# Optimization experiments

Hardware: AMD Instinct MI355X
Metric: run time of the kernel (lower is better)

## Reference

```python
import jax, jax.numpy as jnp
import numpy as np

N_NODES = 50000
N_EDGES = 800000
D_IN = 64
D_OUT = 64
EDGE_DIM = 32
BN_EPS = 1e-5
GIN_EPS = 0.0


def setup_inputs() -> dict:
    key = jax.random.key(0)
    ks = jax.random.split(key, 8)
    x = jax.random.normal(ks[0], (N_NODES, D_IN), dtype=jnp.float32)
    edge_index = jax.random.randint(ks[1], (2, N_EDGES), 0, N_NODES, dtype=jnp.int64)
    edge_attr = jax.random.normal(ks[2], (N_EDGES, EDGE_DIM), dtype=jnp.float32)
    # learned params (scaled like kaiming-ish init)
    We = jax.random.normal(ks[3], (EDGE_DIM, D_IN), dtype=jnp.float32) / np.sqrt(EDGE_DIM)
    be = jnp.zeros((D_IN,), dtype=jnp.float32)
    W1 = jax.random.normal(ks[4], (D_IN, D_OUT), dtype=jnp.float32) / np.sqrt(D_IN)
    b1 = jnp.zeros((D_OUT,), dtype=jnp.float32)
    gamma = jnp.ones((D_OUT,), dtype=jnp.float32)
    beta = jnp.zeros((D_OUT,), dtype=jnp.float32)
    W2 = jax.random.normal(ks[5], (D_OUT, D_OUT), dtype=jnp.float32) / np.sqrt(D_OUT)
    b2 = jnp.zeros((D_OUT,), dtype=jnp.float32)
    return {"x": x, "edge_index": edge_index, "edge_attr": edge_attr,
            "We": We, "be": be, "W1": W1, "b1": b1,
            "gamma": gamma, "beta": beta, "W2": W2, "b2": b2}


def reference(x, edge_index, edge_attr, We, be, W1, b1, gamma, beta, W2, b2):
    src = edge_index[0]  # j (source), PyG default flow source_to_target
    dst = edge_index[1]  # i (target)
    # message: x_j + lin(edge_attr)
    msg = x[src] + (edge_attr @ We + be)              # [E, D_IN]
    # scatter-add aggregate into target nodes
    agg = jax.ops.segment_sum(msg, dst, num_segments=x.shape[0])  # [N, D_IN]
    # GIN residual
    out = agg + (1.0 + GIN_EPS) * x
    # MLP: Linear -> BatchNorm1d (training stats) -> ReLU -> Linear
    h = out @ W1 + b1
    mean = jnp.mean(h, axis=0)
    var = jnp.var(h, axis=0)
    h = (h - mean) * jax.lax.rsqrt(var + BN_EPS) * gamma + beta
    h = jax.nn.relu(h)
    return h @ W2 + b2
```

## Files before the change

### kernel.cpp

```cpp
#include <hip/hip_runtime.h>

#define N_NODES 50000
#define N_EDGES 800000
#define D 64
#define ED 32
#define BN_EPS 1e-5f

#define NBKT 250
#define NPB  200
#define NB_HIST 500
#define EPB  1600

#define WS_SUMS     0
#define WS_SUMSQ    64
#define WS_BTOT     128
#define WS_RESV     384
#define WS_ZERO_END 640
#define WS_OFF      640
#define WS_PACK     50644
#define WS_SRC2     (WS_PACK + 2 * N_EDGES)
#define WS_AGGEA    (WS_SRC2 + 2 * N_EDGES)
#define WS_PRE      (WS_AGGEA + N_NODES * ED)
#define WS_H        (WS_PRE + N_NODES * D)
#define WS_WC       (WS_H + N_NODES * D)
#define WS_BEC      (WS_WC + ED * D)

#define N_BLK ((N_NODES + 63) / 64)

__global__ __launch_bounds__(256) void foldw_kernel(
    const float* __restrict__ We, const float* __restrict__ W1,
    const float* __restrict__ be, float* __restrict__ wc, float* __restrict__ bec)
{
    const int idx = blockIdx.x * 256 + threadIdx.x;
    if (idx < ED * D) {
        const int j = idx >> 6, f = idx & 63;
        float a = 0.f;
        for (int k = 0; k < D; ++k) a += We[j * D + k] * W1[k * D + f];
        wc[idx] = a;
    }
    if (idx < D) {
        float a = 0.f;
        for (int k = 0; k < D; ++k) a += be[k] * W1[k * D + idx];
        bec[idx] = a;
    }
}

__global__ __launch_bounds__(256) void bin_hist_kernel(
    const int* __restrict__ dst, int* __restrict__ btot)
{
    __shared__ int hist[NBKT];
    const int t = threadIdx.x;
    if (t < NBKT) hist[t] = 0;
    __syncthreads();
    const int e0 = blockIdx.x * EPB;
    for (int i = t; i < EPB; i += 256)
        atomicAdd(&hist[dst[e0 + i] / NPB], 1);
    __syncthreads();
    if (t < NBKT) atomicAdd(&btot[t], hist[t]);
}

__global__ __launch_bounds__(256) void bin_scatter_kernel(
    const int* __restrict__ ei, const int* __restrict__ btot,
    int* __restrict__ resv, uint2* __restrict__ pack)
{
    __shared__ int sA[256], sB[256];
    __shared__ int bb[NBKT];
    __shared__ int hist[NBKT], seg[NBKT], lcur[NBKT];
    const int t = threadIdx.x;
    if (t < NBKT) { hist[t] = 0; lcur[t] = 0; }
    sA[t] = (t < NBKT) ? btot[t] : 0;
    __syncthreads();
    int* cur = sA; int* nxt = sB;
    for (int o = 1; o < 256; o <<= 1) {
        nxt[t] = cur[t] + (t >= o ? cur[t - o] : 0);
        __syncthreads();
        int* tmp = cur; cur = nxt; nxt = tmp;
    }
    if (t < NBKT) bb[t] = (t == 0) ? 0 : cur[t - 1];
    __syncthreads();

    const int e0 = blockIdx.x * EPB;
    for (int i = t; i < EPB; i += 256)
        atomicAdd(&hist[ei[N_EDGES + e0 + i] / NPB], 1);
    __syncthreads();
    if (t < NBKT) seg[t] = bb[t] + atomicAdd(&resv[t], hist[t]);
    __syncthreads();
    for (int i = t; i < EPB; i += 256) {
        const int e = e0 + i;
        const int s = ei[e];
        const int d = ei[N_EDGES + e];
        const int bkt = d / NPB;
        const int r = atomicAdd(&lcur[bkt], 1);
        pack[seg[bkt] + r] = make_uint2(((unsigned)d << 16) | (unsigned)s,
                                        (unsigned)e);
    }
}

__global__ __launch_bounds__(512) void bucket_place_kernel(
    const int* __restrict__ btot, const uint2* __restrict__ pack,
    int* __restrict__ off, int2* __restrict__ sorted)
{
    __shared__ int sA[256], sB[256];
    __shared__ int cnt[NPB], lcur[NPB];
    __shared__ int pA[256], pB[256];
    __shared__ int sBase, sNE;
    const int t = threadIdx.x;
    const int j = blockIdx.x;
    if (t < 256) sA[t] = (t < NBKT) ? btot[t] : 0;
    if (t < NPB) { cnt[t] = 0; lcur[t] = 0; }
    __syncthreads();
    int* cur = sA; int* nxt = sB;
    for (int o = 1; o < 256; o <<= 1) {
        if (t < 256) nxt[t] = cur[t] + (t >= o ? cur[t - o] : 0);
        __syncthreads();
        int* tmp = cur; cur = nxt; nxt = tmp;
    }
    if (t == 0) { sBase = (j == 0) ? 0 : cur[j - 1]; sNE = btot[j]; }
    __syncthreads();
    const int base = sBase, nE = sNE;
    const uint2* pp = pack + base;

    for (int i = t; i < nE; i += 512)
        atomicAdd(&cnt[(int)(pp[i].x >> 16) - j * NPB], 1);
    __syncthreads();
    if (t < 256) pA[t] = (t < NPB) ? cnt[t] : 0;
    __syncthreads();
    int* c2 = pA; int* n2 = pB;
    for (int o = 1; o < 256; o <<= 1) {
        if (t < 256) n2[t] = c2[t] + (t >= o ? c2[t - o] : 0);
        __syncthreads();
        int* tmp = c2; c2 = n2; n2 = tmp;
    }
    if (t < NPB) {
        const int excl = (t == 0) ? 0 : c2[t - 1];
        n2[t] = excl;
        off[j * NPB + t] = base + excl;
    }
    if (j == NBKT - 1 && t == 0) off[N_NODES] = N_EDGES;
    __syncthreads();
    for (int i = t; i < nE; i += 512) {
        const uint2 w = pp[i];
        const int dl = (int)(w.x >> 16) - j * NPB;
        const int r = atomicAdd(&lcur[dl], 1);
        sorted[base + n2[dl] + r] = make_int2((int)w.y, (int)(w.x & 0xffffu));
    }
}

__global__ __launch_bounds__(256) void agg_kernel(
    const float* __restrict__ x, const float* __restrict__ ea,
    const int* __restrict__ off, const int2* __restrict__ sorted,
    float* __restrict__ pre, float* __restrict__ aggEA)
{
    const int f = threadIdx.x & 63;
    const int w = threadIdx.x >> 6;
    const int fe = f & 31;
    const bool lo = (f < 32);
    const int nwv = gridDim.x * 4;
    for (int node = blockIdx.x * 4 + w; node < N_NODES; node += nwv) {
        const int start = __builtin_amdgcn_readfirstlane(off[node]);
        const int n     = __builtin_amdgcn_readfirstlane(off[node + 1]) - start;
        const int2* sp = sorted + start;
        float s = x[(size_t)node * D + f];
        float ax = 0.f, ay = 0.f;
        int it = 0;
        if (n >= 8) {
            int2 c0 = sp[0], c1 = sp[1], c2 = sp[2], c3 = sp[3];
            int2 c4 = sp[4], c5 = sp[5], c6 = sp[6], c7 = sp[7];
            for (; it + 16 <= n; it += 8) {
                const int2 n0 = sp[it + 8],  n1 = sp[it + 9];
                const int2 n2 = sp[it + 10], n3 = sp[it + 11];
                const int2 n4 = sp[it + 12], n5 = sp[it + 13];
                const int2 n6 = sp[it + 14], n7 = sp[it + 15];
                s += x[(size_t)c0.y * D + f]; s += x[(size_t)c1.y * D + f];
                s += x[(size_t)c2.y * D + f]; s += x[(size_t)c3.y * D + f];
                s += x[(size_t)c4.y * D + f]; s += x[(size_t)c5.y * D + f];
                s += x[(size_t)c6.y * D + f]; s += x[(size_t)c7.y * D + f];
                ax += ea[(size_t)(lo ? c0.x : c1.x) * ED + fe];
                ax += ea[(size_t)(lo ? c2.x : c3.x) * ED + fe];
                ay += ea[(size_t)(lo ? c4.x : c5.x) * ED + fe];
                ay += ea[(size_t)(lo ? c6.x : c7.x) * ED + fe];
                c0 = n0; c1 = n1; c2 = n2; c3 = n3;
                c4 = n4; c5 = n5; c6 = n6; c7 = n7;
            }
            s += x[(size_t)c0.y * D + f]; s += x[(size_t)c1.y * D + f];
            s += x[(size_t)c2.y * D + f]; s += x[(size_t)c3.y * D + f];
            s += x[(size_t)c4.y * D + f]; s += x[(size_t)c5.y * D + f];
            s += x[(size_t)c6.y * D + f]; s += x[(size_t)c7.y * D + f];
            ax += ea[(size_t)(lo ? c0.x : c1.x) * ED + fe];
            ax += ea[(size_t)(lo ? c2.x : c3.x) * ED + fe];
            ay += ea[(size_t)(lo ? c4.x : c5.x) * ED + fe];
            ay += ea[(size_t)(lo ? c6.x : c7.x) * ED + fe];
            it += 8;
        }
        for (; it < n; ++it) {
            const int2 p = sp[it];
            s += x[(size_t)p.y * D + f];
            if (lo) ax += ea[(size_t)p.x * ED + fe];
        }
        pre[(size_t)node * D + f] = s;
        ax += ay;
        ax += __shfl_xor(ax, 32);
        if (lo) aggEA[(size_t)node * ED + fe] = ax;
    }
}

__global__ __launch_bounds__(256) void mlp1g_kernel(
    const float* __restrict__ pre, const float* __restrict__ aggEA,
    const int* __restrict__ off,
    const float* __restrict__ W1, const float* __restrict__ wc,
    const float* __restrict__ bec, const float* __restrict__ b1,
    float* __restrict__ h, float* __restrict__ sums, float* __restrict__ sumsq)
{
    __shared__ float As[64 * 100];
    __shared__ float Bs[96 * 64];
    __shared__ float4 sb1v[16];
    __shared__ float4 sbecv[16];
    __shared__ float sDeg[64];
    const int tid = threadIdx.x;
    const int base = blockIdx.x * 64;

    for (int i = tid; i < 64 * 16; i += 256)
        ((float4*)Bs)[i] = ((const float4*)W1)[i];
    for (int i = tid; i < 32 * 16; i += 256)
        ((float4*)Bs)[64 * 16 + i] = ((const float4*)wc)[i];
    if (tid < 16)      sb1v[tid] = ((const float4*)b1)[tid];
    else if (tid < 32) sbecv[tid - 16] = ((const float4*)bec)[tid - 16];
    if (tid < 64) {
        const int node = base + tid;
        sDeg[tid] = (node < N_NODES) ? (float)(off[node + 1] - off[node]) : 0.f;
    }
    #pragma unroll
    for (int r = 0; r < 4; ++r) {
        const int idx = tid + 256 * r;
        const int nl = idx >> 4, c4 = idx & 15;
        const bool v = (base + nl) < N_NODES;
        const float4 t = v ? ((const float4*)pre)[(size_t)(base + nl) * 16 + c4]
                           : make_float4(0.f, 0.f, 0.f, 0.f);
        *(float4*)&As[nl * 100 + c4 * 4] = t;
    }
    #pragma unroll
    for (int r = 0; r < 2; ++r) {
        const int idx = tid + 256 * r;
        const int nl = idx >> 3, c4 = idx & 7;
        const bool v = (base + nl) < N_NODES;
        const float4 t = v ? ((const float4*)aggEA)[(size_t)(base + nl) * 8 + c4]
                           : make_float4(0.f, 0.f, 0.f, 0.f);
        *(float4*)&As[nl * 100 + 64 + c4 * 4] = t;
    }
    __syncthreads();

    const int tx = tid & 15, ty = tid >> 4;
    const int r0 = ty * 4;
    const float4 bb = sb1v[tx];
    const float4 bc = sbecv[tx];
    float4 acc0, acc1, acc2, acc3;
    acc0.x = bb.x + sDeg[r0+0]*bc.x; acc0.y = bb.y + sDeg[r0+0]*bc.y;
    acc0.z = bb.z + sDeg[r0+0]*bc.z; acc0.w = bb.w + sDeg[r0+0]*bc.w;
    acc1.x = bb.x + sDeg[r0+1]*bc.x; acc1.y = bb.y + sDeg[r0+1]*bc.y;
    acc1.z = bb.z + sDeg[r0+1]*bc.z; acc1.w = bb.w + sDeg[r0+1]*bc.w;
    acc2.x = bb.x + sDeg[r0+2]*bc.x; acc2.y = bb.y + sDeg[r0+2]*bc.y;
    acc2.z = bb.z + sDeg[r0+2]*bc.z; acc2.w = bb.w + sDeg[r0+2]*bc.w;
    acc3.x = bb.x + sDeg[r0+3]*bc.x; acc3.y = bb.y + sDeg[r0+3]*bc.y;
    acc3.z = bb.z + sDeg[r0+3]*bc.z; acc3.w = bb.w + sDeg[r0+3]*bc.w;

    for (int k4 = 0; k4 < 24; ++k4) {
        const int k = k4 * 4;
        const float4 a0 = *(const float4*)&As[(r0+0)*100 + k];
        const float4 a1 = *(const float4*)&As[(r0+1)*100 + k];
        const float4 a2 = *(const float4*)&As[(r0+2)*100 + k];
        const float4 a3 = *(const float4*)&As[(r0+3)*100 + k];
        const float4 w0 = *(const float4*)&Bs[(k+0)*64 + tx*4];
        const float4 w1v = *(const float4*)&Bs[(k+1)*64 + tx*4];
        const float4 w2v = *(const float4*)&Bs[(k+2)*64 + tx*4];
        const float4 w3v = *(const float4*)&Bs[(k+3)*64 + tx*4];
        acc0.x += a0.x*w0.x + a0.y*w1v.x + a0.z*w2v.x + a0.w*w3v.x;
        acc0.y += a0.x*w0.y + a0.y*w1v.y + a0.z*w2v.y + a0.w*w3v.y;
        acc0.z += a0.x*w0.z + a0.y*w1v.z + a0.z*w2v.z + a0.w*w3v.z;
        acc0.w += a0.x*w0.w + a0.y*w1v.w + a0.z*w2v.w + a0.w*w3v.w;
        acc1.x += a1.x*w0.x + a1.y*w1v.x + a1.z*w2v.x + a1.w*w3v.x;
        acc1.y += a1.x*w0.y + a1.y*w1v.y + a1.z*w2v.y + a1.w*w3v.y;
        acc1.z += a1.x*w0.z + a1.y*w1v.z + a1.z*w2v.z + a1.w*w3v.z;
        acc1.w += a1.x*w0.w + a1.y*w1v.w + a1.z*w2v.w + a1.w*w3v.w;
        acc2.x += a2.x*w0.x + a2.y*w1v.x + a2.z*w2v.x + a2.w*w3v.x;
        acc2.y += a2.x*w0.y + a2.y*w1v.y + a2.z*w2v.y + a2.w*w3v.y;
        acc2.z += a2.x*w0.z + a2.y*w1v.z + a2.z*w2v.z + a2.w*w3v.z;
        acc2.w += a2.x*w0.w + a2.y*w1v.w + a2.z*w2v.w + a2.w*w3v.w;
        acc3.x += a3.x*w0.x + a3.y*w1v.x + a3.z*w2v.x + a3.w*w3v.x;
        acc3.y += a3.x*w0.y + a3.y*w1v.y + a3.z*w2v.y + a3.w*w3v.y;
        acc3.z += a3.x*w0.z + a3.y*w1v.z + a3.z*w2v.z + a3.w*w3v.z;
        acc3.w += a3.x*w0.w + a3.y*w1v.w + a3.z*w2v.w + a3.w*w3v.w;
    }

    float4 ps = make_float4(0.f, 0.f, 0.f, 0.f);
    float4 pq = make_float4(0.f, 0.f, 0.f, 0.f);
    {
        const int n0 = base + r0;
        if (n0 + 0 < N_NODES) {
            ((float4*)h)[(size_t)(n0+0)*16 + tx] = acc0;
            ps.x += acc0.x; ps.y += acc0.y; ps.z += acc0.z; ps.w += acc0.w;
            pq.x += acc0.x*acc0.x; pq.y += acc0.y*acc0.y;
            pq.z += acc0.z*acc0.z; pq.w += acc0.w*acc0.w;
        }
        if (n0 + 1 < N_NODES) {
            ((float4*)h)[(size_t)(n0+1)*16 + tx] = acc1;
            ps.x += acc1.x; ps.y += acc1.y; ps.z += acc1.z; ps.w += acc1.w;
            pq.x += acc1.x*acc1.x; pq.y += acc1.y*acc1.y;
            pq.z += acc1.z*acc1.z; pq.w += acc1.w*acc1.w;
        }
        if (n0 + 2 < N_NODES) {
            ((float4*)h)[(size_t)(n0+2)*16 + tx] = acc2;
            ps.x += acc2.x; ps.y += acc2.y; ps.z += acc2.z; ps.w += acc2.w;
            pq.x += acc2.x*acc2.x; pq.y += acc2.y*acc2.y;
            pq.z += acc2.z*acc2.z; pq.w += acc2.w*acc2.w;
        }
        if (n0 + 3 < N_NODES) {
            ((float4*)h)[(size_t)(n0+3)*16 + tx] = acc3;
            ps.x += acc3.x; ps.y += acc3.y; ps.z += acc3.z; ps.w += acc3.w;
            pq.x += acc3.x*acc3.x; pq.y += acc3.y*acc3.y;
            pq.z += acc3.z*acc3.z; pq.w += acc3.w*acc3.w;
        }
    }
    __syncthreads();
    float* sS = Bs;
    float* sQ = Bs + 1024;
    sS[ty*64 + tx*4 + 0] = ps.x; sS[ty*64 + tx*4 + 1] = ps.y;
    sS[ty*64 + tx*4 + 2] = ps.z; sS[ty*64 + tx*4 + 3] = ps.w;
    sQ[ty*64 + tx*4 + 0] = pq.x; sQ[ty*64 + tx*4 + 1] = pq.y;
    sQ[ty*64 + tx*4 + 2] = pq.z; sQ[ty*64 + tx*4 + 3] = pq.w;
    __syncthreads();
    if (tid < 64) {
        float s = 0.f, q = 0.f;
        #pragma unroll
        for (int r = 0; r < 16; ++r) { s += sS[r*64 + tid]; q += sQ[r*64 + tid]; }
        unsafeAtomicAdd(&sums[tid], s);
        unsafeAtomicAdd(&sumsq[tid], q);
    }
}

__global__ __launch_bounds__(256) void mlp2g_kernel(
    const float* __restrict__ h, const float* __restrict__ W2,
    const float* __restrict__ b2, const float* __restrict__ sums,
    const float* __restrict__ sumsq, const float* __restrict__ gamma,
    const float* __restrict__ beta, float* __restrict__ out)
{
    __shared__ float As[64 * 68];
    __shared__ float Bs[64 * 64];
    __shared__ float4 sb2v[16];
    __shared__ float4 sscv[16];
    __shared__ float4 sshv[16];
    const int tid = threadIdx.x;
    const int base = blockIdx.x * 64;

    for (int i = tid; i < 64 * 16; i += 256)
        ((float4*)Bs)[i] = ((const float4*)W2)[i];
    if (tid < 16) sb2v[tid] = ((const float4*)b2)[tid];
    if (tid < 64) {
        const float inv_n = 1.0f / (float)N_NODES;
        const float mean = sums[tid] * inv_n;
        const float var  = sumsq[tid] * inv_n - mean * mean;
        const float sc   = gamma[tid] * rsqrtf(var + BN_EPS);
        ((float*)sscv)[tid] = sc;
        ((float*)sshv)[tid] = beta[tid] - mean * sc;
    }
    __syncthreads();

    #pragma unroll
    for (int r = 0; r < 4; ++r) {
        const int idx = tid + 256 * r;
        const int nl = idx >> 4, c4 = idx & 15;
        const bool v = (base + nl) < N_NODES;
        const float4 t = v ? ((const float4*)h)[(size_t)(base + nl) * 16 + c4]
                           : make_float4(0.f, 0.f, 0.f, 0.f);
        const float4 c = sscv[c4];
        const float4 s = sshv[c4];
        float4 rv;
        rv.x = fmaxf(t.x * c.x + s.x, 0.f);
        rv.y = fmaxf(t.y * c.y + s.y, 0.f);
        rv.z = fmaxf(t.z * c.z + s.z, 0.f);
        rv.w = fmaxf(t.w * c.w + s.w, 0.f);
        *(float4*)&As[nl * 68 + c4 * 4] = rv;
    }
    __syncthreads();

    const int tx = tid & 15, ty = tid >> 4;
    const int r0 = ty * 4;
    const float4 bb = sb2v[tx];
    float4 acc0 = bb, acc1 = bb, acc2 = bb, acc3 = bb;

    for (int k4 = 0; k4 < 16; ++k4) {
        const int k = k4 * 4;
        const float4 a0 = *(const float4*)&As[(r0+0)*68 + k];
        const float4 a1 = *(const float4*)&As[(r0+1)*68 + k];
        const float4 a2 = *(const float4*)&As[(r0+2)*68 + k];
        const float4 a3 = *(const float4*)&As[(r0+3)*68 + k];
        const float4 w0 = *(const float4*)&Bs[(k+0)*64 + tx*4];
        const float4 w1v = *(const float4*)&Bs[(k+1)*64 + tx*4];
        const float4 w2v = *(const float4*)&Bs[(k+2)*64 + tx*4];
        const float4 w3v = *(const float4*)&Bs[(k+3)*64 + tx*4];
        acc0.x += a0.x*w0.x + a0.y*w1v.x + a0.z*w2v.x + a0.w*w3v.x;
        acc0.y += a0.x*w0.y + a0.y*w1v.y + a0.z*w2v.y + a0.w*w3v.y;
        acc0.z += a0.x*w0.z + a0.y*w1v.z + a0.z*w2v.z + a0.w*w3v.z;
        acc0.w += a0.x*w0.w + a0.y*w1v.w + a0.z*w2v.w + a0.w*w3v.w;
        acc1.x += a1.x*w0.x + a1.y*w1v.x + a1.z*w2v.x + a1.w*w3v.x;
        acc1.y += a1.x*w0.y + a1.y*w1v.y + a1.z*w2v.y + a1.w*w3v.y;
        acc1.z += a1.x*w0.z + a1.y*w1v.z + a1.z*w2v.z + a1.w*w3v.z;
        acc1.w += a1.x*w0.w + a1.y*w1v.w + a1.z*w2v.w + a1.w*w3v.w;
        acc2.x += a2.x*w0.x + a2.y*w1v.x + a2.z*w2v.x + a2.w*w3v.x;
        acc2.y += a2.x*w0.y + a2.y*w1v.y + a2.z*w2v.y + a2.w*w3v.y;
        acc2.z += a2.x*w0.z + a2.y*w1v.z + a2.z*w2v.z + a2.w*w3v.z;
        acc2.w += a2.x*w0.w + a2.y*w1v.w + a2.z*w2v.w + a2.w*w3v.w;
        acc3.x += a3.x*w0.x + a3.y*w1v.x + a3.z*w2v.x + a3.w*w3v.x;
        acc3.y += a3.x*w0.y + a3.y*w1v.y + a3.z*w2v.y + a3.w*w3v.y;
        acc3.z += a3.x*w0.z + a3.y*w1v.z + a3.z*w2v.z + a3.w*w3v.z;
        acc3.w += a3.x*w0.w + a3.y*w1v.w + a3.z*w2v.w + a3.w*w3v.w;
    }

    const int n0 = base + r0;
    if (n0 + 0 < N_NODES) ((float4*)out)[(size_t)(n0+0)*16 + tx] = acc0;
    if (n0 + 1 < N_NODES) ((float4*)out)[(size_t)(n0+1)*16 + tx] = acc1;
    if (n0 + 2 < N_NODES) ((float4*)out)[(size_t)(n0+2)*16 + tx] = acc2;
    if (n0 + 3 < N_NODES) ((float4*)out)[(size_t)(n0+3)*16 + tx] = acc3;
}

extern "C" void kernel_launch(void* const* d_in, const int* in_sizes, int n_in,
                              void* d_out, int out_size, void* d_ws, size_t ws_size,
                              hipStream_t stream) {
    const float* x     = (const float*)d_in[0];
    const int*   ei    = (const int*)  d_in[1];
    const float* ea    = (const float*)d_in[2];
    const float* We    = (const float*)d_in[3];
    const float* be    = (const float*)d_in[4];
    const float* W1    = (const float*)d_in[5];
    const float* b1    = (const float*)d_in[6];
    const float* gamma = (const float*)d_in[7];
    const float* beta  = (const float*)d_in[8];
    const float* W2    = (const float*)d_in[9];
    const float* b2    = (const float*)d_in[10];

    float* ws      = (float*)d_ws;
    float* sums    = ws + WS_SUMS;
    float* sumsq   = ws + WS_SUMSQ;
    int*   btot    = (int*)(ws + WS_BTOT);
    int*   resv    = (int*)(ws + WS_RESV);
    int*   off     = (int*)(ws + WS_OFF);
    uint2* pack    = (uint2*)(ws + WS_PACK);
    int2*  sorted2 = (int2*)(ws + WS_SRC2);
    float* aggEA   = ws + WS_AGGEA;
    float* pre     = ws + WS_PRE;
    float* h       = ws + WS_H;
    float* wcbuf   = ws + WS_WC;
    float* becbuf  = ws + WS_BEC;

    hipMemsetAsync(ws, 0, (size_t)WS_ZERO_END * sizeof(float), stream);

    foldw_kernel       <<<8, 256, 0, stream>>>(We, W1, be, wcbuf, becbuf);
    bin_hist_kernel    <<<NB_HIST, 256, 0, stream>>>(ei + N_EDGES, btot);
    bin_scatter_kernel <<<NB_HIST, 256, 0, stream>>>(ei, btot, resv, pack);
    bucket_place_kernel<<<NBKT, 512, 0, stream>>>(btot, pack, off, sorted2);
    agg_kernel         <<<2048, 256, 0, stream>>>(x, ea, off, sorted2, pre, aggEA);
    mlp1g_kernel       <<<N_BLK, 256, 0, stream>>>(pre, aggEA, off, W1, wcbuf,
                                                   becbuf, b1, h, sums, sumsq);
    mlp2g_kernel       <<<N_BLK, 256, 0, stream>>>(h, W2, b2, sums, sumsq,
                                                   gamma, beta, (float*)d_out);
}
```

Measured before the change: 306.7 us.

## Move edge-attribute aggregation into bucket placement via shared-memory atomics

The edge_attr gather-sum per destination node moves out of agg_kernel and into bucket_place_kernel. That kernel already owns a 200-node bucket, so it accumulates edge_attr rows into a 200x32 shared-memory buffer with float atomics and writes the result out. The sorted edge list shrinks from int2 to plain source indices, which cuts index traffic in agg_kernel and removes its edge_attr gathers. The cost is heavy LDS atomic contention, only 250 blocks doing 800K×32 atomic adds, and float summation order that now varies from run to run.

```diff
diff --git a/kernel.cpp b/kernel.cpp
--- a/kernel.cpp
+++ b/kernel.cpp
@@ -18,8 +18,8 @@
 #define WS_ZERO_END 640
 #define WS_OFF      640
 #define WS_PACK     50644
-#define WS_SRC2     (WS_PACK + 2 * N_EDGES)
-#define WS_AGGEA    (WS_SRC2 + 2 * N_EDGES)
+#define WS_SRC      (WS_PACK + 2 * N_EDGES)
+#define WS_AGGEA    (WS_SRC + N_EDGES)
 #define WS_PRE      (WS_AGGEA + N_NODES * ED)
 #define WS_H        (WS_PRE + N_NODES * D)
 #define WS_WC       (WS_H + N_NODES * D)
@@ -98,16 +98,19 @@
 
 __global__ __launch_bounds__(512) void bucket_place_kernel(
     const int* __restrict__ btot, const uint2* __restrict__ pack,
-    int* __restrict__ off, int2* __restrict__ sorted)
+    const float* __restrict__ ea,
+    int* __restrict__ off, int* __restrict__ ssrc, float* __restrict__ aggEA)
 {
     __shared__ int sA[256], sB[256];
     __shared__ int cnt[NPB], lcur[NPB];
     __shared__ int pA[256], pB[256];
+    __shared__ float sEA[NPB * ED];
     __shared__ int sBase, sNE;
     const int t = threadIdx.x;
     const int j = blockIdx.x;
     if (t < 256) sA[t] = (t < NBKT) ? btot[t] : 0;
     if (t < NPB) { cnt[t] = 0; lcur[t] = 0; }
+    for (int i = t; i < NPB * ED; i += 512) sEA[i] = 0.f;
     __syncthreads();
     int* cur = sA; int* nxt = sB;
     for (int o = 1; o < 256; o <<= 1) {
@@ -138,69 +141,65 @@
     }
     if (j == NBKT - 1 && t == 0) off[N_NODES] = N_EDGES;
     __syncthreads();
-    for (int i = t; i < nE; i += 512) {
+
+    const int g = t >> 3, sub = t & 7;
+    for (int i = g; i < nE; i += 64) {
         const uint2 w = pp[i];
         const int dl = (int)(w.x >> 16) - j * NPB;
-        const int r = atomicAdd(&lcur[dl], 1);
-        sorted[base + n2[dl] + r] = make_int2((int)w.y, (int)(w.x & 0xffffu));
-    }
+        if (sub == 0) {
+            const int r = atomicAdd(&lcur[dl], 1);
+            ssrc[base + n2[dl] + r] = (int)(w.x & 0xffffu);
+        }
+        const float4 v = ((const float4*)ea)[(size_t)w.y * 8 + sub];
+        float* p = &sEA[dl * ED + sub * 4];
+        atomicAdd(p + 0, v.x);
+        atomicAdd(p + 1, v.y);
+        atomicAdd(p + 2, v.z);
+        atomicAdd(p + 3, v.w);
+    }
+    __syncthreads();
+    float4* dst4 = (float4*)(aggEA + (size_t)j * NPB * ED);
+    for (int i = t; i < NPB * (ED / 4); i += 512)
+        dst4[i] = ((const float4*)sEA)[i];
 }
 
 __global__ __launch_bounds__(256) void agg_kernel(
-    const float* __restrict__ x, const float* __restrict__ ea,
-    const int* __restrict__ off, const int2* __restrict__ sorted,
-    float* __restrict__ pre, float* __restrict__ aggEA)
+    const float* __restrict__ x, const int* __restrict__ off,
+    const int* __restrict__ ssrc, float* __restrict__ pre)
 {
     const int f = threadIdx.x & 63;
     const int w = threadIdx.x >> 6;
-    const int fe = f & 31;
-    const bool lo = (f < 32);
     const int nwv = gridDim.x * 4;
     for (int node = blockIdx.x * 4 + w; node < N_NODES; node += nwv) {
         const int start = __builtin_amdgcn_readfirstlane(off[node]);
         const int n     = __builtin_amdgcn_readfirstlane(off[node + 1]) - start;
-        const int2* sp = sorted + start;
+        const int* sp = ssrc + start;
         float s = x[(size_t)node * D + f];
-        float ax = 0.f, ay = 0.f;
         int it = 0;
         if (n >= 8) {
-            int2 c0 = sp[0], c1 = sp[1], c2 = sp[2], c3 = sp[3];
-            int2 c4 = sp[4], c5 = sp[5], c6 = sp[6], c7 = sp[7];
+            int c0 = sp[0], c1 = sp[1], c2 = sp[2], c3 = sp[3];
+            int c4 = sp[4], c5 = sp[5], c6 = sp[6], c7 = sp[7];
             for (; it + 16 <= n; it += 8) {
-                const int2 n0 = sp[it + 8],  n1 = sp[it + 9];
-                const int2 n2 = sp[it + 10], n3 = sp[it + 11];
-                const int2 n4 = sp[it + 12], n5 = sp[it + 13];
-                const int2 n6 = sp[it + 14], n7 = sp[it + 15];
-                s += x[(size_t)c0.y * D + f]; s += x[(size_t)c1.y * D + f];
-                s += x[(size_t)c2.y * D + f]; s += x[(size_t)c3.y * D + f];
-                s += x[(size_t)c4.y * D + f]; s += x[(size_t)c5.y * D + f];
-                s += x[(size_t)c6.y * D + f]; s += x[(size_t)c7.y * D + f];
-                ax += ea[(size_t)(lo ? c0.x : c1.x) * ED + fe];
-                ax += ea[(size_t)(lo ? c2.x : c3.x) * ED + fe];
-                ay += ea[(size_t)(lo ? c4.x : c5.x) * ED + fe];
-                ay += ea[(size_t)(lo ? c6.x : c7.x) * ED + fe];
+                const int n0 = sp[it + 8],  n1 = sp[it + 9];
+                const int n2 = sp[it + 10], n3 = sp[it + 11];
+                const int n4 = sp[it + 12], n5 = sp[it + 13];
+                const int n6 = sp[it + 14], n7 = sp[it + 15];
+                s += x[(size_t)c0 * D + f]; s += x[(size_t)c1 * D + f];
+                s += x[(size_t)c2 * D + f]; s += x[(size_t)c3 * D + f];
+                s += x[(size_t)c4 * D + f]; s += x[(size_t)c5 * D + f];
+                s += x[(size_t)c6 * D + f]; s += x[(size_t)c7 * D + f];
                 c0 = n0; c1 = n1; c2 = n2; c3 = n3;
                 c4 = n4; c5 = n5; c6 = n6; c7 = n7;
             }
-            s += x[(size_t)c0.y * D + f]; s += x[(size_t)c1.y * D + f];
-            s += x[(size_t)c2.y * D + f]; s += x[(size_t)c3.y * D + f];
-            s += x[(size_t)c4.y * D + f]; s += x[(size_t)c5.y * D + f];
-            s += x[(size_t)c6.y * D + f]; s += x[(size_t)c7.y * D + f];
-            ax += ea[(size_t)(lo ? c0.x : c1.x) * ED + fe];
-            ax += ea[(size_t)(lo ? c2.x : c3.x) * ED + fe];
-            ay += ea[(size_t)(lo ? c4.x : c5.x) * ED + fe];
-            ay += ea[(size_t)(lo ? c6.x : c7.x) * ED + fe];
+            s += x[(size_t)c0 * D + f]; s += x[(size_t)c1 * D + f];
+            s += x[(size_t)c2 * D + f]; s += x[(size_t)c3 * D + f];
+            s += x[(size_t)c4 * D + f]; s += x[(size_t)c5 * D + f];
+            s += x[(size_t)c6 * D + f]; s += x[(size_t)c7 * D + f];
             it += 8;
         }
-        for (; it < n; ++it) {
-            const int2 p = sp[it];
-            s += x[(size_t)p.y * D + f];
-            if (lo) ax += ea[(size_t)p.x * ED + fe];
-        }
+        for (; it < n; ++it)
+            s += x[(size_t)sp[it] * D + f];
         pre[(size_t)node * D + f] = s;
-        ax += ay;
-        ax += __shfl_xor(ax, 32);
-        if (lo) aggEA[(size_t)node * ED + fe] = ax;
     }
 }
 
@@ -444,7 +443,7 @@
     int*   resv    = (int*)(ws + WS_RESV);
     int*   off     = (int*)(ws + WS_OFF);
     uint2* pack    = (uint2*)(ws + WS_PACK);
-    int2*  sorted2 = (int2*)(ws + WS_SRC2);
+    int*   ssrc    = (int*)(ws + WS_SRC);
     float* aggEA   = ws + WS_AGGEA;
     float* pre     = ws + WS_PRE;
     float* h       = ws + WS_H;
@@ -456,8 +455,8 @@
     foldw_kernel       <<<8, 256, 0, stream>>>(We, W1, be, wcbuf, becbuf);
     bin_hist_kernel    <<<NB_HIST, 256, 0, stream>>>(ei + N_EDGES, btot);
     bin_scatter_kernel <<<NB_HIST, 256, 0, stream>>>(ei, btot, resv, pack);
-    bucket_place_kernel<<<NBKT, 512, 0, stream>>>(btot, pack, off, sorted2);
-    agg_kernel         <<<2048, 256, 0, stream>>>(x, ea, off, sorted2, pre, aggEA);
+    bucket_place_kernel<<<NBKT, 512, 0, stream>>>(btot, pack, ea, off, ssrc, aggEA);
+    agg_kernel         <<<2048, 256, 0, stream>>>(x, off, ssrc, pre);
     mlp1g_kernel       <<<N_BLK, 256, 0, stream>>>(pre, aggEA, off, W1, wcbuf,
                                                    becbuf, b1, h, sums, sumsq);
     mlp2g_kernel       <<<N_BLK, 256, 0, stream>>>(h, W2, b2, sums, sumsq,
```

After: 411.9 us. 34.3% more time.
